# Performance work log

Hardware: AMD Instinct MI355X
Metric: run time of the kernel (lower is better)

The kernel has to match this reference:

```python
import jax, jax.numpy as jnp
import numpy as np
from jax import lax

BITS = 8  # w_p = a_p = 8 (HAWQ int8)

def _round_ste(x):
    # straight-through round (quant-aware training semantics)
    return x + lax.stop_gradient(jnp.round(x) - x)

def _quant_act(x):
    # QuantAct: symmetric per-tensor activation fake-quant; returns (quantized x, scale)
    n = 2.0 ** (BITS - 1) - 1.0
    sf = jnp.maximum(jnp.max(jnp.abs(x)) / n, 1e-8)
    q = jnp.clip(_round_ste(x / sf), -n, n)
    return q * sf, sf

def _quant_conv(x, w, b, pre_sf, stride, pad):
    # QuantConv2d: per-output-channel symmetric weight quant, integer conv on
    # x/pre_sf with rounded weights, rescale by pre_sf * w_sf. Bias quantized at
    # combined scale. Returns (float output, w_sf) for scale propagation.
    n = 2.0 ** (BITS - 1) - 1.0
    w_sf = jnp.maximum(jnp.max(jnp.abs(w), axis=(1, 2, 3)) / n, 1e-8)
    w_int = _round_ste(w / w_sf[:, None, None, None])
    b_sf = w_sf * pre_sf
    b_int = _round_ste(b / b_sf)
    y = lax.conv_general_dilated(x / pre_sf, w_int, (stride, stride),
                                 [(pad, pad), (pad, pad)],
                                 dimension_numbers=('NCHW', 'OIHW', 'NCHW'))
    return (y + b_int[None, :, None, None]) * b_sf[None, :, None, None], w_sf

def _bn(x, g, b, m, v, eps=1e-5):
    # BatchNorm2d in eval mode (running stats), folded into scale/shift
    inv = g / jnp.sqrt(v + eps)
    return x * inv[None, :, None, None] + (b - m * inv)[None, :, None, None]

def _quant_linear(x, w, b, pre_sf):
    # QuantLinear: per-output-row symmetric weight quant
    n = 2.0 ** (BITS - 1) - 1.0
    w_sf = jnp.maximum(jnp.max(jnp.abs(w), axis=1) / n, 1e-8)
    w_int = _round_ste(w / w_sf[:, None])
    b_sf = w_sf * pre_sf
    b_int = _round_ste(b / b_sf)
    return ((x / pre_sf) @ w_int.T + b_int[None, :]) * b_sf[None, :]

def _forward(x, w0, b0, g0, bb0, m0, v0, w1, b1, g1, bb1, m1, v1,
             w2, b2, g2, bb2, m2, v2, w3, b3, g3, bb3, m3, v3,
             w4, b4, g4, bb4, m4, v4, wd, bd):
    x, psf = _quant_act(x)
    x, _ = _quant_conv(x, w0, b0, psf, 1, 1)   # [B,32,32,32]
    x = _bn(x, g0, bb0, m0, v0)
    x, psf = _quant_act(x)
    x, _ = _quant_conv(x, w1, b1, psf, 1, 0)   # 1x1 -> [B,4,32,32]
    x = _bn(x, g1, bb1, m1, v1)
    x, psf = _quant_act(x)
    x, _ = _quant_conv(x, w2, b2, psf, 2, 1)   # [B,32,16,16]
    x = _bn(x, g2, bb2, m2, v2)
    x, psf = _quant_act(x)
    x, _ = _quant_conv(x, w3, b3, psf, 2, 1)   # [B,32,8,8]
    x = _bn(x, g3, bb3, m3, v3)
    x, psf = _quant_act(x)
    x, _ = _quant_conv(x, w4, b4, psf, 1, 1)   # [B,32,8,8]
    x = _bn(x, g4, bb4, m4, v4)
    x, psf = _quant_act(x)
    x = x.reshape(-1, 2048)                    # 32*8*8 = 2048
    x = _quant_linear(x, wd, bd, psf)          # [B,10]
    return jax.nn.softmax(x, axis=0)           # dim=0 as in original module

def setup_inputs() -> dict:
    key = jax.random.key(0)
    ks = jax.random.split(key, 40)
    B = 1024
    inp = {"x": jax.random.normal(ks[0], (B, 3, 32, 32), jnp.float32)}
    conv_shapes = [(32, 3, 3, 3), (4, 32, 1, 1), (32, 4, 3, 3), (32, 32, 3, 3), (32, 32, 3, 3)]
    for i, s in enumerate(conv_shapes):
        c = s[0]
        inp[f"w{i}"] = jax.random.normal(ks[1 + i], s, jnp.float32) * 0.1
        inp[f"b{i}"] = jax.random.normal(ks[6 + i], (c,), jnp.float32) * 0.01
        inp[f"g{i}"] = 1.0 + 0.1 * jax.random.normal(ks[11 + i], (c,), jnp.float32)
        inp[f"bb{i}"] = 0.1 * jax.random.normal(ks[16 + i], (c,), jnp.float32)
        inp[f"m{i}"] = 0.1 * jax.random.normal(ks[21 + i], (c,), jnp.float32)
        inp[f"v{i}"] = 0.5 + jax.random.uniform(ks[26 + i], (c,), jnp.float32)
    inp["wd"] = jax.random.normal(ks[31], (10, 2048), jnp.float32) * 0.05
    inp["bd"] = jnp.zeros((10,), jnp.float32)
    return inp

def reference(x, w0, b0, g0, bb0, m0, v0, w1, b1, g1, bb1, m1, v1,
              w2, b2, g2, bb2, m2, v2, w3, b3, g3, bb3, m3, v3,
              w4, b4, g4, bb4, m4, v4, wd, bd):
    return _forward(x, w0, b0, g0, bb0, m0, v0, w1, b1, g1, bb1, m1, v1,
                    w2, b2, g2, bb2, m2, v2, w3, b3, g3, bb3, m3, v3,
                    w4, b4, g4, bb4, m4, v4, wd, bd)
```

## Files before the change

### kernel.cpp

```cpp
#include <hip/hip_runtime.h>

#define DI __device__ __forceinline__

constexpr int OFF_WSF0 = 384;
constexpr int OFF_BNS0 = 416;
constexpr int OFF_BNB0 = 448;
constexpr int OFF_W0I  = 480;
constexpr int OFF_WSF1 = 1344;
constexpr int OFF_BNS1 = 1348;
constexpr int OFF_BNB1 = 1352;
constexpr int OFF_W1I  = 1356;
constexpr int OFF_WSF2 = 1484;
constexpr int OFF_BNS2 = 1516;
constexpr int OFF_BNB2 = 1548;
constexpr int OFF_W2I  = 1580;
constexpr int OFF_WSF3 = 2732;
constexpr int OFF_BNS3 = 2764;
constexpr int OFF_BNB3 = 2796;
constexpr int OFF_W3I  = 2828;
constexpr int OFF_WSF4 = 12044;
constexpr int OFF_BNS4 = 12076;
constexpr int OFF_BNB4 = 12108;
constexpr int OFF_W4I  = 12140;
constexpr int OFF_WSFD = 21356;
constexpr int OFF_WDI  = 21368;
constexpr int OFF_LOG  = 41856;
constexpr int OFF_ACT  = 52224;
constexpr long ACT_A_OFF = OFF_ACT;
constexpr long ACT_B_OFF = OFF_ACT + 8388608L;

DI float quantv(float x, float sf) {
    float q = rintf(x / sf);
    return fminf(fmaxf(q, -127.0f), 127.0f);
}
DI float get_sf(const unsigned* umax, int slot) {
    const unsigned* p = umax + slot * 64;
    unsigned m = 0u;
    #pragma unroll
    for (int i = 0; i < 64; ++i) m = m > p[i] ? m : p[i];
    return fmaxf(__uint_as_float(m) / 127.0f, 1e-8f);
}
DI void block_max_atomic(float v, unsigned* dst) {
    __shared__ float redm_[4];
    #pragma unroll
    for (int o = 32; o; o >>= 1) v = fmaxf(v, __shfl_down(v, o, 64));
    int wid = threadIdx.x >> 6;
    if ((threadIdx.x & 63) == 0) redm_[wid] = v;
    __syncthreads();
    if (threadIdx.x == 0) {
        int nw = blockDim.x >> 6;
        float m = redm_[0];
        for (int i = 1; i < nw; ++i) m = fmaxf(m, redm_[i]);
        atomicMax(dst + (blockIdx.x & 63), __float_as_uint(m));
    }
}

struct PrepEntry {
    const float *w, *g, *bb, *m, *v;
    float *wsf, *wint, *bns, *bnb;
    int K; int has_bn;
};
struct PrepAll { PrepEntry e[6]; unsigned* umax; };

__global__ __launch_bounds__(256) void k_prep_all(PrepAll pa) {
    int blk = blockIdx.x;
    if (blk == 142) {
        for (int i = threadIdx.x; i < 384; i += 256) pa.umax[i] = 0u;
        return;
    }
    int layer, oc;
    if      (blk < 32)  { layer = 0; oc = blk; }
    else if (blk < 36)  { layer = 1; oc = blk - 32; }
    else if (blk < 68)  { layer = 2; oc = blk - 36; }
    else if (blk < 100) { layer = 3; oc = blk - 68; }
    else if (blk < 132) { layer = 4; oc = blk - 100; }
    else                { layer = 5; oc = blk - 132; }
    PrepEntry a = pa.e[layer];
    const float* wr = a.w + (long)oc * a.K;
    float mx = 0.f;
    for (int i = threadIdx.x; i < a.K; i += 256) mx = fmaxf(mx, fabsf(wr[i]));
    __shared__ float red[4];
    __shared__ float s_sf;
    #pragma unroll
    for (int o = 32; o; o >>= 1) mx = fmaxf(mx, __shfl_down(mx, o, 64));
    if ((threadIdx.x & 63) == 0) red[threadIdx.x >> 6] = mx;
    __syncthreads();
    if (threadIdx.x == 0) {
        float t = fmaxf(fmaxf(red[0], red[1]), fmaxf(red[2], red[3]));
        t = fmaxf(t / 127.0f, 1e-8f);
        a.wsf[oc] = t; s_sf = t;
        if (a.has_bn) {
            float inv = a.g[oc] / sqrtf(a.v[oc] + 1e-5f);
            a.bns[oc] = inv;
            a.bnb[oc] = a.bb[oc] - a.m[oc] * inv;
        }
    }
    __syncthreads();
    float sf = s_sf;
    for (int i = threadIdx.x; i < a.K; i += 256) a.wint[(long)oc * a.K + i] = rintf(wr[i] / sf);
}

__global__ __launch_bounds__(256) void k_absmax(const float4* __restrict__ x, int n4, unsigned* dst) {
    float m = 0.f;
    for (int i = blockIdx.x * blockDim.x + threadIdx.x; i < n4; i += gridDim.x * blockDim.x) {
        float4 t = x[i];
        m = fmaxf(m, fmaxf(fmaxf(fabsf(t.x), fabsf(t.y)), fmaxf(fabsf(t.z), fabsf(t.w))));
    }
    block_max_atomic(m, dst);
}

__global__ __launch_bounds__(256) void k_conv0maxN(
    const float* __restrict__ x, const float* __restrict__ w0i,
    const float* __restrict__ wsf0, const float* __restrict__ bias0,
    const float* __restrict__ bns0, const float* __restrict__ bnb0,
    const unsigned* __restrict__ umax, unsigned* __restrict__ mout) {
    __shared__ float tile[3 * 18 * 36];
    __shared__ float wlds[27 * 32];
    __shared__ float As[32], Cs[32];
    const int b  = blockIdx.x >> 1;
    const int r0 = (blockIdx.x & 1) * 16;
    const int tid = threadIdx.x;
    const float sfx = get_sf(umax, 0);
    if (tid < 32) {
        int oc = tid;
        float bsf = wsf0[oc] * sfx;
        float bint = rintf(bias0[oc] / bsf);
        float a = bsf * bns0[oc];
        As[oc] = a;
        Cs[oc] = fmaf(bint, a, bnb0[oc]);
    }
    for (int i = tid; i < 1944; i += 256) tile[i] = 0.f;
    for (int i = tid; i < 864; i += 256) {
        int k = i >> 5, oc = i & 31;
        wlds[i] = w0i[oc * 27 + k];
    }
    __syncthreads();
    const float* xb = x + (long)b * 3072;
    for (int i = tid; i < 1728; i += 256) {
        int ci = i / 576, rem = i - ci * 576;
        int rr = rem >> 5, cc = rem & 31;
        int gr = r0 - 1 + rr;
        if ((unsigned)gr < 32u)
            tile[ci * 648 + rr * 36 + cc + 1] = quantv(xb[ci * 1024 + gr * 32 + cc], sfx);
    }
    __syncthreads();
    const int oc0  = (tid >> 5) * 4;
    const int pxg  = tid & 31;
    const int row  = pxg >> 1;
    const int wcol = (pxg & 1) * 16;
    float acc[4][16];
    #pragma unroll
    for (int o = 0; o < 4; ++o)
        #pragma unroll
        for (int p = 0; p < 16; ++p) acc[o][p] = 0.f;
    #pragma unroll 1
    for (int kk = 0; kk < 9; ++kk) {
        int ci = kk / 3, ky = kk - ci * 3;
        const float* rp = tile + ci * 648 + (row + ky) * 36 + wcol;
        float wn[20];
        #pragma unroll
        for (int d = 0; d < 5; ++d) *(float4*)&wn[4 * d] = *(const float4*)&rp[4 * d];
        #pragma unroll
        for (int kx = 0; kx < 3; ++kx) {
            float4 wv = *(const float4*)&wlds[(kk * 3 + kx) * 32 + oc0];
            const float* wf = &wv.x;
            #pragma unroll
            for (int o = 0; o < 4; ++o)
                #pragma unroll
                for (int p = 0; p < 16; ++p)
                    acc[o][p] = fmaf(wn[p + kx], wf[o], acc[o][p]);
        }
    }
    float lmax = 0.f;
    #pragma unroll
    for (int o = 0; o < 4; ++o) {
        float A = As[oc0 + o], C = Cs[oc0 + o];
        #pragma unroll
        for (int p = 0; p < 16; ++p)
            lmax = fmaxf(lmax, fabsf(fmaf(acc[o][p], A, C)));
    }
    block_max_atomic(lmax, mout);
}

__global__ __launch_bounds__(256) void k_conv01n(
    const float* __restrict__ x, const float* __restrict__ w0i,
    const float* __restrict__ wsf0, const float* __restrict__ bias0,
    const float* __restrict__ bns0, const float* __restrict__ bnb0,
    const float* __restrict__ w1i,
    const float* __restrict__ wsf1, const float* __restrict__ bias1,
    const float* __restrict__ bns1, const float* __restrict__ bnb1,
    const unsigned* __restrict__ umax, unsigned* __restrict__ mout,
    float* __restrict__ out) {
    __shared__ float tile[1944];
    __shared__ float wls0[896];
    __shared__ float wls1[128];
    __shared__ float As[32], Cs[32];
    __shared__ float A1s[4], C1s[4];
    const int b  = blockIdx.x >> 1;
    const int r0 = (blockIdx.x & 1) * 16;
    const int tid = threadIdx.x;
    const float sfx = get_sf(umax, 0);
    const float sf1 = get_sf(umax, 1);
    if (tid < 32) {
        int oc = tid;
        float bsf = wsf0[oc] * sfx;
        float bint = rintf(bias0[oc] / bsf);
        float a = bsf * bns0[oc];
        As[oc] = a;
        Cs[oc] = fmaf(bint, a, bnb0[oc]);
    }
    if (tid >= 64 && tid < 68) {
        int oc = tid - 64;
        float bsf = wsf1[oc] * sf1;
        float bint = rintf(bias1[oc] / bsf);
        float a = bsf * bns1[oc];
        A1s[oc] = a;
        C1s[oc] = fmaf(bint, a, bnb1[oc]);
    }
    for (int i = tid; i < 1944; i += 256) tile[i] = 0.f;
    for (int i = tid; i < 864; i += 256) {
        int oc = i / 27, k = i - oc * 27;
        wls0[oc * 28 + k] = w0i[i];
    }
    if (tid >= 128 && tid < 256) {
        int j = tid - 128;
        wls1[(j & 31) * 4 + (j >> 5)] = w1i[j];
    }
    __syncthreads();
    const float* xb = x + (long)b * 3072;
    for (int i = tid; i < 1728; i += 256) {
        int ci = i / 576, rem = i - ci * 576;
        int rr = rem >> 5, cc = rem & 31;
        int gr = r0 - 1 + rr;
        if ((unsigned)gr < 32u)
            tile[ci * 648 + rr * 36 + cc + 1] = quantv(xb[ci * 1024 + gr * 32 + cc], sfx);
    }
    __syncthreads();
    const int h   = tid >> 4;
    const int w0c = (tid & 15) * 2;
    float win[3][3][4];
    #pragma unroll
    for (int ci = 0; ci < 3; ++ci)
        #pragma unroll
        for (int ky = 0; ky < 3; ++ky) {
            const int base = ci * 648 + (h + ky) * 36 + w0c;
            #pragma unroll
            for (int d = 0; d < 4; ++d) win[ci][ky][d] = tile[base + d];
        }
    float acc1[4][2];
    #pragma unroll
    for (int o = 0; o < 4; ++o) { acc1[o][0] = 0.f; acc1[o][1] = 0.f; }
    #pragma unroll 1
    for (int oc = 0; oc < 32; ++oc) {
        float wreg[28];
        const float4* wp4 = (const float4*)&wls0[oc * 28];
        #pragma unroll
        for (int d = 0; d < 7; ++d) *(float4*)&wreg[4 * d] = wp4[d];
        float a0 = 0.f, a1 = 0.f;
        #pragma unroll
        for (int ci = 0; ci < 3; ++ci)
            #pragma unroll
            for (int ky = 0; ky < 3; ++ky)
                #pragma unroll
                for (int kx = 0; kx < 3; ++kx) {
                    float wv = wreg[ci * 9 + ky * 3 + kx];
                    a0 = fmaf(win[ci][ky][kx],     wv, a0);
                    a1 = fmaf(win[ci][ky][kx + 1], wv, a1);
                }
        float A = As[oc], C = Cs[oc];
        float q0 = quantv(fmaf(a0, A, C), sf1);
        float q1 = quantv(fmaf(a1, A, C), sf1);
        const float4 w1v = *(const float4*)&wls1[oc * 4];
        acc1[0][0] = fmaf(q0, w1v.x, acc1[0][0]); acc1[0][1] = fmaf(q1, w1v.x, acc1[0][1]);
        acc1[1][0] = fmaf(q0, w1v.y, acc1[1][0]); acc1[1][1] = fmaf(q1, w1v.y, acc1[1][1]);
        acc1[2][0] = fmaf(q0, w1v.z, acc1[2][0]); acc1[2][1] = fmaf(q1, w1v.z, acc1[2][1]);
        acc1[3][0] = fmaf(q0, w1v.w, acc1[3][0]); acc1[3][1] = fmaf(q1, w1v.w, acc1[3][1]);
    }
    float lmax = 0.f;
    float* ob = out + (long)b * 4096 + (r0 + h) * 32 + w0c;
    #pragma unroll
    for (int o = 0; o < 4; ++o) {
        float y0 = fmaf(acc1[o][0], A1s[o], C1s[o]);
        float y1 = fmaf(acc1[o][1], A1s[o], C1s[o]);
        lmax = fmaxf(lmax, fmaxf(fabsf(y0), fabsf(y1)));
        float2 r2; r2.x = y0; r2.y = y1;
        *(float2*)&ob[o * 1024] = r2;
    }
    block_max_atomic(lmax, mout);
}

__global__ __launch_bounds__(256) void k_conv2c(
    const float* __restrict__ inp, const float* __restrict__ wgl,
    const float* __restrict__ wsf, const float* __restrict__ bias,
    const float* __restrict__ bns, const float* __restrict__ bnb,
    const unsigned* __restrict__ umax, unsigned* __restrict__ mout,
    float* __restrict__ out) {
    __shared__ float tile[4 * 34 * 36];
    __shared__ float wlds[36 * 32];
    __shared__ float As[32], Cs[32];
    const int tid = threadIdx.x;
    const float sf = get_sf(umax, 2);
    if (tid < 32) {
        int oc = tid;
        float bsf = wsf[oc] * sf;
        float bint = rintf(bias[oc] / bsf);
        float a = bsf * bns[oc];
        As[oc] = a;
        Cs[oc] = fmaf(bint, a, bnb[oc]);
    }
    for (int i = tid; i < 4896; i += 256) tile[i] = 0.f;
    for (int i = tid; i < 1152; i += 256) {
        int k = i >> 5, oc = i & 31;
        wlds[i] = wgl[oc * 36 + k];
    }
    __syncthreads();
    const float* ib = inp + (long)blockIdx.x * 4096;
    for (int i = tid; i < 4096; i += 256) {
        int ci = i >> 10, px = i & 1023;
        int iy = px >> 5, ix = px & 31;
        tile[ci * 1224 + (iy + 1) * 36 + (ix + 1)] = quantv(ib[i], sf);
    }
    __syncthreads();
    const int oc0 = (tid >> 6) * 8;
    const int pxq = tid & 63;
    const int h = pxq >> 2, c = pxq & 3;
    float acc[8][4];
    #pragma unroll
    for (int k = 0; k < 8; ++k)
        #pragma unroll
        for (int p = 0; p < 4; ++p) acc[k][p] = 0.f;
    #pragma unroll 1
    for (int ci = 0; ci < 4; ++ci) {
        #pragma unroll
        for (int ky = 0; ky < 3; ++ky) {
            const float* rp = tile + ci * 1224 + (2 * h + ky) * 36 + 8 * c;
            float wn[12];
            #pragma unroll
            for (int d = 0; d < 3; ++d) *(float4*)&wn[4 * d] = *(const float4*)&rp[4 * d];
            #pragma unroll
            for (int kx = 0; kx < 3; ++kx) {
                const float* wp = &wlds[(ci * 9 + ky * 3 + kx) * 32 + oc0];
                float4 wa = *(const float4*)&wp[0];
                float4 wb = *(const float4*)&wp[4];
                float wf[8] = {wa.x, wa.y, wa.z, wa.w, wb.x, wb.y, wb.z, wb.w};
                #pragma unroll
                for (int k = 0; k < 8; ++k)
                    #pragma unroll
                    for (int p = 0; p < 4; ++p)
                        acc[k][p] = fmaf(wn[2 * p + kx], wf[k], acc[k][p]);
            }
        }
    }
    float lmax = 0.f;
    float* ob = out + (long)blockIdx.x * 8192;
    #pragma unroll
    for (int k = 0; k < 8; ++k) {
        int oc = oc0 + k;
        float A = As[oc], C = Cs[oc];
        float4 r;
        float* rp = &r.x;
        #pragma unroll
        for (int p = 0; p < 4; ++p) {
            float y = fmaf(acc[k][p], A, C);
            rp[p] = y;
            lmax = fmaxf(lmax, fabsf(y));
        }
        *(float4*)&ob[oc * 256 + h * 16 + c * 4] = r;
    }
    block_max_atomic(lmax, mout);
}

template<int HIN, int S>
__global__ __launch_bounds__(256) void k_conv34b(
    const float* __restrict__ inp, const float* __restrict__ wi,
    const float* __restrict__ wsf, const float* __restrict__ bias,
    const float* __restrict__ bns, const float* __restrict__ bnb,
    const unsigned* __restrict__ umax, int slot, unsigned* __restrict__ mout,
    float* __restrict__ out) {
    constexpr int ROWS = HIN + 2;
    constexpr int RS   = (S == 2) ? 20 : 12;
    constexpr int TI   = 8 * ROWS * RS;
    constexpr int PIX  = HIN * HIN;
    constexpr int NELT = 2 * 8 * PIX;
    constexpr int WINW = (S == 2) ? 12 : 8;
    constexpr int ND   = (S == 2) ? 3 : 2;
    __shared__ float tile[2 * TI];
    __shared__ float wlds[72 * 36];
    __shared__ float As[32], Cs[32];
    const int tid  = threadIdx.x;
    const int imgl = tid >> 7;
    const int ocg  = (tid >> 4) & 7;
    const int pxq  = tid & 15;
    const int h = pxq >> 1, c = pxq & 1;
    const float sf = get_sf(umax, slot);
    if (tid < 32) {
        int oc = tid;
        float bsf = wsf[oc] * sf;
        float bint = rintf(bias[oc] / bsf);
        float a = bsf * bns[oc];
        As[oc] = a;
        Cs[oc] = fmaf(bint, a, bnb[oc]);
    }
    for (int i = tid; i < 2 * TI; i += 256) tile[i] = 0.f;
    float acc[16];
    #pragma unroll
    for (int i = 0; i < 16; ++i) acc[i] = 0.f;
    const float* ib = inp + (long)blockIdx.x * 2 * 32 * PIX;
    for (int ph = 0; ph < 4; ++ph) {
        __syncthreads();
        for (int i = tid; i < NELT; i += 256) {
            int im = i / (8 * PIX);
            int r  = i % (8 * PIX);
            int ci = r / PIX;
            int px = r % PIX;
            int iy = px / HIN, ix = px % HIN;
            tile[(im * 8 + ci) * (ROWS * RS) + (iy + 1) * RS + (ix + 1)] =
                quantv(ib[(long)(im * 32 + ph * 8 + ci) * PIX + px], sf);
        }
        for (int i = tid; i < 2304; i += 256) {
            int oc = i / 72, k = i - oc * 72;
            wlds[k * 36 + oc] = wi[oc * 288 + ph * 72 + k];
        }
        __syncthreads();
        const float* tb = tile + imgl * TI;
        #pragma unroll 2
        for (int ci = 0; ci < 8; ++ci) {
            float win[3][WINW];
            #pragma unroll
            for (int ky = 0; ky < 3; ++ky) {
                const float* rp = tb + ci * (ROWS * RS) + (S * h + ky) * RS + S * 4 * c;
                #pragma unroll
                for (int d = 0; d < ND; ++d)
                    *(float4*)&win[ky][4 * d] = *(const float4*)&rp[4 * d];
            }
            #pragma unroll
            for (int ky = 0; ky < 3; ++ky)
                #pragma unroll
                for (int kx = 0; kx < 3; ++kx) {
                    int j = ky * 3 + kx;
                    float4 wv = *(const float4*)&wlds[(ci * 9 + j) * 36 + ocg * 4];
                    float wvf[4] = {wv.x, wv.y, wv.z, wv.w};
                    #pragma unroll
                    for (int k = 0; k < 4; ++k)
                        #pragma unroll
                        for (int px = 0; px < 4; ++px)
                            acc[k * 4 + px] = fmaf(win[ky][S * px + kx], wvf[k], acc[k * 4 + px]);
                }
        }
    }
    float lmax = 0.f;
    long imgg = (long)blockIdx.x * 2 + imgl;
    #pragma unroll
    for (int k = 0; k < 4; ++k) {
        int oc = ocg * 4 + k;
        float A = As[oc], C = Cs[oc];
        float4 r;
        float* rp = &r.x;
        #pragma unroll
        for (int px = 0; px < 4; ++px) {
            float y = fmaf(acc[k * 4 + px], A, C);
            rp[px] = y;
            lmax = fmaxf(lmax, fabsf(y));
        }
        *(float4*)&out[(imgg * 32 + oc) * 64 + h * 8 + c * 4] = r;
    }
    block_max_atomic(lmax, mout);
}

__global__ __launch_bounds__(256) void k_fc(
    const float* __restrict__ act, const float* __restrict__ wdi,
    const float* __restrict__ wsfd, const float* __restrict__ bd,
    const unsigned* __restrict__ umax, float* __restrict__ logits) {
    int b = blockIdx.x;
    float sf = get_sf(umax, 5);
    const float* ab = act + (long)b * 2048;
    float acc[10];
    #pragma unroll
    for (int c = 0; c < 10; ++c) acc[c] = 0.f;
    #pragma unroll
    for (int k = 0; k < 8; ++k) {
        int j = threadIdx.x + 256 * k;
        float q = quantv(ab[j], sf);
        #pragma unroll
        for (int c = 0; c < 10; ++c) acc[c] = fmaf(q, wdi[c * 2048 + j], acc[c]);
    }
    #pragma unroll
    for (int c = 0; c < 10; ++c)
        #pragma unroll
        for (int o = 32; o; o >>= 1) acc[c] += __shfl_down(acc[c], o, 64);
    __shared__ float red[4][10];
    int wid = threadIdx.x >> 6;
    if ((threadIdx.x & 63) == 0)
        #pragma unroll
        for (int c = 0; c < 10; ++c) red[wid][c] = acc[c];
    __syncthreads();
    if (threadIdx.x < 10) {
        int c = threadIdx.x;
        float s = red[0][c] + red[1][c] + red[2][c] + red[3][c];
        float bsf = wsfd[c] * sf;
        float bint = rintf(bd[c] / bsf);
        logits[b * 10 + c] = (s + bint) * bsf;
    }
}

__global__ __launch_bounds__(256) void k_softmax(const float* __restrict__ logits, float* __restrict__ out) {
    int c = blockIdx.x;
    float v0 = logits[(threadIdx.x +   0) * 10 + c];
    float v1 = logits[(threadIdx.x + 256) * 10 + c];
    float v2 = logits[(threadIdx.x + 512) * 10 + c];
    float v3 = logits[(threadIdx.x + 768) * 10 + c];
    float mx = fmaxf(fmaxf(v0, v1), fmaxf(v2, v3));
    __shared__ float redm[4];
    __shared__ float reds[4];
    #pragma unroll
    for (int o = 32; o; o >>= 1) mx = fmaxf(mx, __shfl_down(mx, o, 64));
    if ((threadIdx.x & 63) == 0) redm[threadIdx.x >> 6] = mx;
    __syncthreads();
    mx = fmaxf(fmaxf(redm[0], redm[1]), fmaxf(redm[2], redm[3]));
    float e0 = expf(v0 - mx), e1 = expf(v1 - mx), e2 = expf(v2 - mx), e3 = expf(v3 - mx);
    float s = (e0 + e1) + (e2 + e3);
    #pragma unroll
    for (int o = 32; o; o >>= 1) s += __shfl_down(s, o, 64);
    if ((threadIdx.x & 63) == 0) reds[threadIdx.x >> 6] = s;
    __syncthreads();
    s = reds[0] + reds[1] + reds[2] + reds[3];
    out[(threadIdx.x +   0) * 10 + c] = e0 / s;
    out[(threadIdx.x + 256) * 10 + c] = e1 / s;
    out[(threadIdx.x + 512) * 10 + c] = e2 / s;
    out[(threadIdx.x + 768) * 10 + c] = e3 / s;
}

extern "C" void kernel_launch(void* const* d_in, const int* in_sizes, int n_in,
                              void* d_out, int out_size, void* d_ws, size_t ws_size,
                              hipStream_t stream) {
    (void)in_sizes; (void)n_in; (void)out_size; (void)ws_size;
    const float* x = (const float*)d_in[0];
    const float *w[5], *bia[5], *g[5], *bb[5], *m[5], *v[5];
    for (int i = 0; i < 5; ++i) {
        w[i]   = (const float*)d_in[1 + 6 * i + 0];
        bia[i] = (const float*)d_in[1 + 6 * i + 1];
        g[i]   = (const float*)d_in[1 + 6 * i + 2];
        bb[i]  = (const float*)d_in[1 + 6 * i + 3];
        m[i]   = (const float*)d_in[1 + 6 * i + 4];
        v[i]   = (const float*)d_in[1 + 6 * i + 5];
    }
    const float* wd = (const float*)d_in[31];
    const float* bd = (const float*)d_in[32];
    float* ws = (float*)d_ws;
    unsigned* umax = (unsigned*)ws;
    float* out = (float*)d_out;

    float* wsf0 = ws + OFF_WSF0; float* bns0 = ws + OFF_BNS0; float* bnb0 = ws + OFF_BNB0; float* w0i = ws + OFF_W0I;
    float* wsf1 = ws + OFF_WSF1; float* bns1 = ws + OFF_BNS1; float* bnb1 = ws + OFF_BNB1; float* w1i = ws + OFF_W1I;
    float* wsf2 = ws + OFF_WSF2; float* bns2 = ws + OFF_BNS2; float* bnb2 = ws + OFF_BNB2; float* w2i = ws + OFF_W2I;
    float* wsf3 = ws + OFF_WSF3; float* bns3 = ws + OFF_BNS3; float* bnb3 = ws + OFF_BNB3; float* w3i = ws + OFF_W3I;
    float* wsf4 = ws + OFF_WSF4; float* bns4 = ws + OFF_BNS4; float* bnb4 = ws + OFF_BNB4; float* w4i = ws + OFF_W4I;
    float* wsfd = ws + OFF_WSFD; float* wdi = ws + OFF_WDI;
    float* logits = ws + OFF_LOG;
    float* actA = ws + ACT_A_OFF;
    float* actB = ws + ACT_B_OFF;

    PrepAll pa;
    pa.umax = umax;
    const float* ww[6] = {w[0], w[1], w[2], w[3], w[4], wd};
    float* wsfp[6] = {wsf0, wsf1, wsf2, wsf3, wsf4, wsfd};
    float* wip[6]  = {w0i, w1i, w2i, w3i, w4i, wdi};
    float* bnsp[6] = {bns0, bns1, bns2, bns3, bns4, nullptr};
    float* bnbp[6] = {bnb0, bnb1, bnb2, bnb3, bnb4, nullptr};
    int Ks[6] = {27, 32, 36, 288, 288, 2048};
    for (int i = 0; i < 6; ++i) {
        pa.e[i].w = ww[i];
        pa.e[i].g = (i < 5) ? g[i] : nullptr;
        pa.e[i].bb = (i < 5) ? bb[i] : nullptr;
        pa.e[i].m = (i < 5) ? m[i] : nullptr;
        pa.e[i].v = (i < 5) ? v[i] : nullptr;
        pa.e[i].wsf = wsfp[i];
        pa.e[i].wint = wip[i];
        pa.e[i].bns = bnsp[i];
        pa.e[i].bnb = bnbp[i];
        pa.e[i].K = Ks[i];
        pa.e[i].has_bn = (i < 5) ? 1 : 0;
    }

    hipLaunchKernelGGL(k_prep_all, dim3(143), dim3(256), 0, stream, pa);
    hipLaunchKernelGGL(k_absmax, dim3(1024), dim3(256), 0, stream,
                       (const float4*)x, 1024 * 3 * 32 * 32 / 4, umax + 0 * 64);
    hipLaunchKernelGGL(k_conv0maxN, dim3(2048), dim3(256), 0, stream,
                       x, w0i, wsf0, bia[0], bns0, bnb0, umax, umax + 1 * 64);
    hipLaunchKernelGGL(k_conv01n, dim3(2048), dim3(256), 0, stream,
                       x, w0i, wsf0, bia[0], bns0, bnb0,
                       w1i, wsf1, bia[1], bns1, bnb1, umax, umax + 2 * 64, actB);
    hipLaunchKernelGGL(k_conv2c, dim3(1024), dim3(256), 0, stream,
                       actB, w2i, wsf2, bia[2], bns2, bnb2, umax, umax + 3 * 64, actA);
    hipLaunchKernelGGL((k_conv34b<16, 2>), dim3(512), dim3(256), 0, stream,
                       actA, w3i, wsf3, bia[3], bns3, bnb3, umax, 3, umax + 4 * 64, actB);
    hipLaunchKernelGGL((k_conv34b<8, 1>),  dim3(512), dim3(256), 0, stream,
                       actB, w4i, wsf4, bia[4], bns4, bnb4, umax, 4, umax + 5 * 64, actA);
    hipLaunchKernelGGL(k_fc, dim3(1024), dim3(256), 0, stream, actA, wdi, wsfd, bd, umax, logits);
    hipLaunchKernelGGL(k_softmax, dim3(10), dim3(256), 0, stream, logits, out);
}
```

Before: 185.2 us.

## Use one image per block in conv3/4 and multiply by reciprocal scale

The conv3/conv4 kernel is restructured so each block handles one image instead of two. Each thread now computes 4 channels by 2 pixels instead of 4 by 4, and the grid is doubled to 1024 blocks. This raises parallelism and cuts registers per thread, but lowers weight reuse per LDS load and trades float4 window loads for scalar ones. Separately, quantization divisions are replaced by multiplication with a precomputed reciprocal, and conv1's requant scale is folded into the BN constants. That can change rounding slightly at tie boundaries.

```diff
diff --git a/kernel.cpp b/kernel.cpp
--- a/kernel.cpp
+++ b/kernel.cpp
@@ -29,8 +29,8 @@
 constexpr long ACT_A_OFF = OFF_ACT;
 constexpr long ACT_B_OFF = OFF_ACT + 8388608L;
 
-DI float quantv(float x, float sf) {
-    float q = rintf(x / sf);
+DI float quantm(float x, float rsf) {
+    float q = rintf(x * rsf);
     return fminf(fmaxf(q, -127.0f), 127.0f);
 }
 DI float get_sf(const unsigned* umax, int slot) {
@@ -121,6 +121,7 @@
     const int r0 = (blockIdx.x & 1) * 16;
     const int tid = threadIdx.x;
     const float sfx = get_sf(umax, 0);
+    const float rsfx = 1.0f / sfx;
     if (tid < 32) {
         int oc = tid;
         float bsf = wsf0[oc] * sfx;
@@ -141,7 +142,7 @@
         int rr = rem >> 5, cc = rem & 31;
         int gr = r0 - 1 + rr;
         if ((unsigned)gr < 32u)
-            tile[ci * 648 + rr * 36 + cc + 1] = quantv(xb[ci * 1024 + gr * 32 + cc], sfx);
+            tile[ci * 648 + rr * 36 + cc + 1] = quantm(xb[ci * 1024 + gr * 32 + cc], rsfx);
     }
     __syncthreads();
     const int oc0  = (tid >> 5) * 4;
@@ -194,20 +195,23 @@
     __shared__ float tile[1944];
     __shared__ float wls0[896];
     __shared__ float wls1[128];
-    __shared__ float As[32], Cs[32];
+    __shared__ float Aq[32], Cq[32];
     __shared__ float A1s[4], C1s[4];
     const int b  = blockIdx.x >> 1;
     const int r0 = (blockIdx.x & 1) * 16;
     const int tid = threadIdx.x;
     const float sfx = get_sf(umax, 0);
+    const float rsfx = 1.0f / sfx;
     const float sf1 = get_sf(umax, 1);
+    const float rsf1 = 1.0f / sf1;
     if (tid < 32) {
         int oc = tid;
         float bsf = wsf0[oc] * sfx;
         float bint = rintf(bias0[oc] / bsf);
         float a = bsf * bns0[oc];
-        As[oc] = a;
-        Cs[oc] = fmaf(bint, a, bnb0[oc]);
+        float c = fmaf(bint, a, bnb0[oc]);
+        Aq[oc] = a * rsf1;
+        Cq[oc] = c * rsf1;
     }
     if (tid >= 64 && tid < 68) {
         int oc = tid - 64;
@@ -233,7 +237,7 @@
         int rr = rem >> 5, cc = rem & 31;
         int gr = r0 - 1 + rr;
         if ((unsigned)gr < 32u)
-            tile[ci * 648 + rr * 36 + cc + 1] = quantv(xb[ci * 1024 + gr * 32 + cc], sfx);
+            tile[ci * 648 + rr * 36 + cc + 1] = quantm(xb[ci * 1024 + gr * 32 + cc], rsfx);
     }
     __syncthreads();
     const int h   = tid >> 4;
@@ -267,9 +271,9 @@
                     a0 = fmaf(win[ci][ky][kx],     wv, a0);
                     a1 = fmaf(win[ci][ky][kx + 1], wv, a1);
                 }
-        float A = As[oc], C = Cs[oc];
-        float q0 = quantv(fmaf(a0, A, C), sf1);
-        float q1 = quantv(fmaf(a1, A, C), sf1);
+        float A = Aq[oc], C = Cq[oc];
+        float q0 = fminf(fmaxf(rintf(fmaf(a0, A, C)), -127.0f), 127.0f);
+        float q1 = fminf(fmaxf(rintf(fmaf(a1, A, C)), -127.0f), 127.0f);
         const float4 w1v = *(const float4*)&wls1[oc * 4];
         acc1[0][0] = fmaf(q0, w1v.x, acc1[0][0]); acc1[0][1] = fmaf(q1, w1v.x, acc1[0][1]);
         acc1[1][0] = fmaf(q0, w1v.y, acc1[1][0]); acc1[1][1] = fmaf(q1, w1v.y, acc1[1][1]);
@@ -300,6 +304,7 @@
     __shared__ float As[32], Cs[32];
     const int tid = threadIdx.x;
     const float sf = get_sf(umax, 2);
+    const float rsf = 1.0f / sf;
     if (tid < 32) {
         int oc = tid;
         float bsf = wsf[oc] * sf;
@@ -318,7 +323,7 @@
     for (int i = tid; i < 4096; i += 256) {
         int ci = i >> 10, px = i & 1023;
         int iy = px >> 5, ix = px & 31;
-        tile[ci * 1224 + (iy + 1) * 36 + (ix + 1)] = quantv(ib[i], sf);
+        tile[ci * 1224 + (iy + 1) * 36 + (ix + 1)] = quantm(ib[i], rsf);
     }
     __syncthreads();
     const int oc0 = (tid >> 6) * 8;
@@ -371,7 +376,7 @@
 }
 
 template<int HIN, int S>
-__global__ __launch_bounds__(256) void k_conv34b(
+__global__ __launch_bounds__(256) void k_conv34c(
     const float* __restrict__ inp, const float* __restrict__ wi,
     const float* __restrict__ wsf, const float* __restrict__ bias,
     const float* __restrict__ bns, const float* __restrict__ bnb,
@@ -381,18 +386,17 @@
     constexpr int RS   = (S == 2) ? 20 : 12;
     constexpr int TI   = 8 * ROWS * RS;
     constexpr int PIX  = HIN * HIN;
-    constexpr int NELT = 2 * 8 * PIX;
-    constexpr int WINW = (S == 2) ? 12 : 8;
-    constexpr int ND   = (S == 2) ? 3 : 2;
-    __shared__ float tile[2 * TI];
+    constexpr int NELT = 8 * PIX;
+    constexpr int WINW = S + 3;
+    __shared__ float tile[TI];
     __shared__ float wlds[72 * 36];
     __shared__ float As[32], Cs[32];
-    const int tid  = threadIdx.x;
-    const int imgl = tid >> 7;
-    const int ocg  = (tid >> 4) & 7;
-    const int pxq  = tid & 15;
-    const int h = pxq >> 1, c = pxq & 1;
+    const int tid = threadIdx.x;
+    const int ocg = tid >> 5;
+    const int pxq = tid & 31;
+    const int h = pxq >> 2, c = pxq & 3;
     const float sf = get_sf(umax, slot);
+    const float rsf = 1.0f / sf;
     if (tid < 32) {
         int oc = tid;
         float bsf = wsf[oc] * sf;
@@ -401,37 +405,33 @@
         As[oc] = a;
         Cs[oc] = fmaf(bint, a, bnb[oc]);
     }
-    for (int i = tid; i < 2 * TI; i += 256) tile[i] = 0.f;
-    float acc[16];
-    #pragma unroll
-    for (int i = 0; i < 16; ++i) acc[i] = 0.f;
-    const float* ib = inp + (long)blockIdx.x * 2 * 32 * PIX;
+    for (int i = tid; i < TI; i += 256) tile[i] = 0.f;
+    float acc[4][2];
+    #pragma unroll
+    for (int k = 0; k < 4; ++k) { acc[k][0] = 0.f; acc[k][1] = 0.f; }
+    const float* ib = inp + (long)blockIdx.x * 32 * PIX;
     for (int ph = 0; ph < 4; ++ph) {
         __syncthreads();
         for (int i = tid; i < NELT; i += 256) {
-            int im = i / (8 * PIX);
-            int r  = i % (8 * PIX);
-            int ci = r / PIX;
-            int px = r % PIX;
-            int iy = px / HIN, ix = px % HIN;
-            tile[(im * 8 + ci) * (ROWS * RS) + (iy + 1) * RS + (ix + 1)] =
-                quantv(ib[(long)(im * 32 + ph * 8 + ci) * PIX + px], sf);
+            int ci = i / PIX;
+            int px = i - ci * PIX;
+            int iy = px / HIN, ix = px & (HIN - 1);
+            tile[ci * (ROWS * RS) + (iy + 1) * RS + (ix + 1)] =
+                quantm(ib[(long)(ph * 8 + ci) * PIX + px], rsf);
         }
         for (int i = tid; i < 2304; i += 256) {
             int oc = i / 72, k = i - oc * 72;
             wlds[k * 36 + oc] = wi[oc * 288 + ph * 72 + k];
         }
         __syncthreads();
-        const float* tb = tile + imgl * TI;
         #pragma unroll 2
         for (int ci = 0; ci < 8; ++ci) {
             float win[3][WINW];
             #pragma unroll
             for (int ky = 0; ky < 3; ++ky) {
-                const float* rp = tb + ci * (ROWS * RS) + (S * h + ky) * RS + S * 4 * c;
+                const int base = ci * (ROWS * RS) + (S * h + ky) * RS + S * 2 * c;
                 #pragma unroll
-                for (int d = 0; d < ND; ++d)
-                    *(float4*)&win[ky][4 * d] = *(const float4*)&rp[4 * d];
+                for (int d = 0; d < WINW; ++d) win[ky][d] = tile[base + d];
             }
             #pragma unroll
             for (int ky = 0; ky < 3; ++ky)
@@ -439,30 +439,24 @@
                 for (int kx = 0; kx < 3; ++kx) {
                     int j = ky * 3 + kx;
                     float4 wv = *(const float4*)&wlds[(ci * 9 + j) * 36 + ocg * 4];
-                    float wvf[4] = {wv.x, wv.y, wv.z, wv.w};
-                    #pragma unroll
-                    for (int k = 0; k < 4; ++k)
-                        #pragma unroll
-                        for (int px = 0; px < 4; ++px)
-                            acc[k * 4 + px] = fmaf(win[ky][S * px + kx], wvf[k], acc[k * 4 + px]);
+                    float x0 = win[ky][kx], x1 = win[ky][S + kx];
+                    acc[0][0] = fmaf(x0, wv.x, acc[0][0]); acc[0][1] = fmaf(x1, wv.x, acc[0][1]);
+                    acc[1][0] = fmaf(x0, wv.y, acc[1][0]); acc[1][1] = fmaf(x1, wv.y, acc[1][1]);
+                    acc[2][0] = fmaf(x0, wv.z, acc[2][0]); acc[2][1] = fmaf(x1, wv.z, acc[2][1]);
+                    acc[3][0] = fmaf(x0, wv.w, acc[3][0]); acc[3][1] = fmaf(x1, wv.w, acc[3][1]);
                 }
         }
     }
     float lmax = 0.f;
-    long imgg = (long)blockIdx.x * 2 + imgl;
     #pragma unroll
     for (int k = 0; k < 4; ++k) {
         int oc = ocg * 4 + k;
         float A = As[oc], C = Cs[oc];
-        float4 r;
-        float* rp = &r.x;
-        #pragma unroll
-        for (int px = 0; px < 4; ++px) {
-            float y = fmaf(acc[k * 4 + px], A, C);
-            rp[px] = y;
-            lmax = fmaxf(lmax, fabsf(y));
-        }
-        *(float4*)&out[(imgg * 32 + oc) * 64 + h * 8 + c * 4] = r;
+        float y0 = fmaf(acc[k][0], A, C);
+        float y1 = fmaf(acc[k][1], A, C);
+        lmax = fmaxf(lmax, fmaxf(fabsf(y0), fabsf(y1)));
+        float2 r2; r2.x = y0; r2.y = y1;
+        *(float2*)&out[((long)blockIdx.x * 32 + oc) * 64 + h * 8 + c * 2] = r2;
     }
     block_max_atomic(lmax, mout);
 }
@@ -473,6 +467,7 @@
     const unsigned* __restrict__ umax, float* __restrict__ logits) {
     int b = blockIdx.x;
     float sf = get_sf(umax, 5);
+    float rsf = 1.0f / sf;
     const float* ab = act + (long)b * 2048;
     float acc[10];
     #pragma unroll
@@ -480,7 +475,7 @@
     #pragma unroll
     for (int k = 0; k < 8; ++k) {
         int j = threadIdx.x + 256 * k;
-        float q = quantv(ab[j], sf);
+        float q = quantm(ab[j], rsf);
         #pragma unroll
         for (int c = 0; c < 10; ++c) acc[c] = fmaf(q, wdi[c * 2048 + j], acc[c]);
     }
@@ -592,9 +587,9 @@
                        w1i, wsf1, bia[1], bns1, bnb1, umax, umax + 2 * 64, actB);
     hipLaunchKernelGGL(k_conv2c, dim3(1024), dim3(256), 0, stream,
                        actB, w2i, wsf2, bia[2], bns2, bnb2, umax, umax + 3 * 64, actA);
-    hipLaunchKernelGGL((k_conv34b<16, 2>), dim3(512), dim3(256), 0, stream,
+    hipLaunchKernelGGL((k_conv34c<16, 2>), dim3(1024), dim3(256), 0, stream,
                        actA, w3i, wsf3, bia[3], bns3, bnb3, umax, 3, umax + 4 * 64, actB);
-    hipLaunchKernelGGL((k_conv34b<8, 1>),  dim3(512), dim3(256), 0, stream,
+    hipLaunchKernelGGL((k_conv34c<8, 1>),  dim3(1024), dim3(256), 0, stream,
                        actB, w4i, wsf4, bia[4], bns4, bnb4, umax, 4, umax + 5 * 64, actA);
     hipLaunchKernelGGL(k_fc, dim3(1024), dim3(256), 0, stream, actA, wdi, wsfd, bd, umax, logits);
     hipLaunchKernelGGL(k_softmax, dim3(10), dim3(256), 0, stream, logits, out);
```

After: 184.7 us. Within noise of the previous version (-0.2%).
